# Optimization experiments

Measured on AMD Instinct MI355X. Metric: run time of the kernel, lower is better.

## Reference

```python
import jax, jax.numpy as jnp
import numpy as np

B, S, D = 4, 2048, 2048
H, NOPE, ROPE, V, KVR = 16, 128, 64, 128, 512
QK = NOPE + ROPE  # 192
THETA = 10000.0
EPS = 1e-6


def setup_inputs() -> dict:
    key = jax.random.key(0)
    ks = jax.random.split(key, 6)
    x = jax.random.normal(ks[0], (B, S, D), jnp.float32)
    wq = jax.random.normal(ks[1], (H * QK, D), jnp.float32) * 0.02
    wkv_a = jax.random.normal(ks[2], (KVR + ROPE, D), jnp.float32) * 0.02
    kv_norm_w = jnp.ones((KVR,), jnp.float32)
    wkv_b = jax.random.normal(ks[3], (H * (NOPE + V), KVR), jnp.float32) * 0.02
    wo = jax.random.normal(ks[4], (D, H * V), jnp.float32) * 0.02
    # rotary frequency tables (interleaved-pair convention, pairs = ROPE//2)
    pos = np.arange(S, dtype=np.float64)
    inv = 1.0 / (THETA ** (np.arange(0, ROPE, 2, dtype=np.float64) / ROPE))
    ang = pos[:, None] * inv[None, :]  # [S, ROPE//2]
    freqs_cos = jnp.asarray(np.cos(ang), jnp.float32)
    freqs_sin = jnp.asarray(np.sin(ang), jnp.float32)
    return dict(x=x, wq=wq, wkv_a=wkv_a, kv_norm_w=kv_norm_w,
                wkv_b=wkv_b, wo=wo, freqs_cos=freqs_cos, freqs_sin=freqs_sin)


def _rope(x, cos, sin):
    # x: [B, S, H, d] with interleaved complex pairs along last dim
    x1, x2 = x[..., 0::2], x[..., 1::2]
    c = cos[None, :, None, :]
    s = sin[None, :, None, :]
    y1 = x1 * c - x2 * s
    y2 = x1 * s + x2 * c
    return jnp.stack([y1, y2], axis=-1).reshape(x.shape)


def _rmsnorm(x, w):
    var = jnp.mean(jnp.square(x), axis=-1, keepdims=True)
    return x * jax.lax.rsqrt(var + EPS) * w


def reference(x, wq, wkv_a, kv_norm_w, wkv_b, wo, freqs_cos, freqs_sin):
    softmax_scale = QK ** (-0.5)  # mscale path inactive (S <= original_seq_len)
    # query projection (q_lora_rank == 0 -> direct)
    q = (x @ wq.T).reshape(B, S, H, QK)
    q_nope, q_pe = q[..., :NOPE], q[..., NOPE:]
    q_pe = _rope(q_pe, freqs_cos, freqs_sin)
    # latent KV projection + decoupled rope key
    kv = x @ wkv_a.T  # [B, S, KVR + ROPE]
    kv_c = _rmsnorm(kv[..., :KVR], kv_norm_w)  # latent KV cache entries
    k_pe = _rope(kv[..., None, KVR:], freqs_cos, freqs_sin)[:, :, 0]  # [B,S,ROPE]
    # absorb wkv_b's nope block into q (attention runs in 512-dim latent space)
    wkv_b_r = wkv_b.reshape(H, NOPE + V, KVR)
    q_lat = jnp.einsum('bshd,hdc->bshc', q_nope, wkv_b_r[:, :NOPE])
    scores = (jnp.einsum('bshc,btc->bsht', q_lat, kv_c)
              + jnp.einsum('bshr,btr->bsht', q_pe, k_pe)) * softmax_scale
    mask = jnp.triu(jnp.full((S, S), -1e9, jnp.float32), k=1)  # causal
    attn = jax.nn.softmax(scores + mask[None, :, None, :], axis=-1)
    out = jnp.einsum('bsht,btc->bshc', attn, kv_c)  # latent output
    out = jnp.einsum('bshc,hdc->bshd', out, wkv_b_r[:, NOPE:])  # un-absorb V
    return out.reshape(B, S, H * V) @ wo.T
```

## Files before the change

### kernel.cpp

```cpp
#include <hip/hip_runtime.h>
#include <hip/hip_bf16.h>
#include <cstdint>

typedef __bf16 bf16;
typedef __bf16 bf16x8 __attribute__((ext_vector_type(8)));
typedef float f32x4 __attribute__((ext_vector_type(4)));
typedef unsigned int u32x4 __attribute__((ext_vector_type(4)));

#define B_ 4
#define S_ 2048
#define D_ 2048
#define H_ 16
#define NOPE_ 128
#define ROPE_ 64
#define V_ 128
#define KVR_ 512
#define QK_ 192
#define KD_ 576

__device__ __forceinline__ bf16 tobf(float f) {
  unsigned u = __float_as_uint(f);
  u += 0x7fffu + ((u >> 16) & 1u);
  unsigned short s = (unsigned short)(u >> 16);
  return *reinterpret_cast<bf16*>(&s);
}
__device__ __forceinline__ float tof(bf16 v) {
  unsigned short s = *reinterpret_cast<unsigned short*>(&v);
  return __uint_as_float(((unsigned)s) << 16);
}

__global__ void cast_bf16(const float* __restrict__ in, bf16* __restrict__ out, long n) {
  long i = ((long)blockIdx.x * 256 + threadIdx.x) * 8;
  if (i >= n) return;
  float4 a = *(const float4*)(in + i);
  float4 b = *(const float4*)(in + i + 4);
  bf16x8 v;
  v[0] = tobf(a.x); v[1] = tobf(a.y); v[2] = tobf(a.z); v[3] = tobf(a.w);
  v[4] = tobf(b.x); v[5] = tobf(b.y); v[6] = tobf(b.z); v[7] = tobf(b.w);
  *(bf16x8*)(out + i) = v;
}

__global__ void prep_wkvb(const float* __restrict__ w, bf16* __restrict__ wnT, bf16* __restrict__ wv) {
  int tid = blockIdx.x * 256 + threadIdx.x;
  {
    int c = tid & 511, rest = tid >> 9, d = rest & 127, h = rest >> 7;
    wv[tid] = tobf(w[((long)(h * 256 + 128 + d) << 9) + c]);
  }
  {
    int d = tid & 127, rest = tid >> 7, c = rest & 511, h = rest >> 9;
    wnT[tid] = tobf(w[((long)(h * 256 + d) << 9) + c]);
  }
}

template <typename OutT>
__global__ __launch_bounds__(256)
void gemm_bt(const bf16* __restrict__ A, long lda, long aOffZ,
             const bf16* __restrict__ Bm, long ldb, long bOffZ,
             OutT* __restrict__ C, long ldc, long cOffZ,
             int M, int N, int K)
{
  A += aOffZ * blockIdx.z;
  Bm += bOffZ * blockIdx.z;
  C += cOffZ * blockIdx.z;
  const int m0 = blockIdx.y * 128, n0 = blockIdx.x * 128;
  const int tid = threadIdx.x;
  const int wave = tid >> 6, lane = tid & 63, quad = lane >> 4, r = lane & 15;
  const int wm = (wave >> 1) * 64, wn = (wave & 1) * 64;
  __shared__ __align__(16) bf16 As[128][40];
  __shared__ __align__(16) bf16 Bs[128][40];
  f32x4 acc[4][4] = {};
  for (int k0 = 0; k0 < K; k0 += 32) {
    __syncthreads();
#pragma unroll
    for (int it = 0; it < 2; ++it) {
      int idx = tid + it * 256;
      int row = idx >> 2, ch = (idx & 3) * 8;
      long ar = m0 + row; if (ar > (long)M - 1) ar = M - 1;
      *(u32x4*)&As[row][ch] = *(const u32x4*)(A + ar * lda + k0 + ch);
      long br = n0 + row; if (br > (long)N - 1) br = N - 1;
      *(u32x4*)&Bs[row][ch] = *(const u32x4*)(Bm + br * ldb + k0 + ch);
    }
    __syncthreads();
    bf16x8 af[4], bfr[4];
#pragma unroll
    for (int i = 0; i < 4; ++i) af[i] = *(const bf16x8*)&As[wm + i * 16 + r][quad * 8];
#pragma unroll
    for (int j = 0; j < 4; ++j) bfr[j] = *(const bf16x8*)&Bs[wn + j * 16 + r][quad * 8];
#pragma unroll
    for (int i = 0; i < 4; ++i)
#pragma unroll
      for (int j = 0; j < 4; ++j)
        acc[i][j] = __builtin_amdgcn_mfma_f32_16x16x32_bf16(af[i], bfr[j], acc[i][j], 0, 0, 0);
  }
#pragma unroll
  for (int i = 0; i < 4; ++i) {
    int mrow = m0 + wm + i * 16 + quad * 4;
#pragma unroll
    for (int j = 0; j < 4; ++j) {
      int ncol = n0 + wn + j * 16 + r;
      if (ncol < N) {
#pragma unroll
        for (int t = 0; t < 4; ++t) {
          if (mrow + t < M) {
            if constexpr (__is_same(OutT, float))
              C[(long)(mrow + t) * ldc + ncol] = acc[i][j][t];
            else
              C[(long)(mrow + t) * ldc + ncol] = tobf(acc[i][j][t]);
          }
        }
      }
    }
  }
}

__global__ void kv_norm(const float* __restrict__ kvf, const float* __restrict__ w,
                        const float* __restrict__ fcos, const float* __restrict__ fsin,
                        bf16* __restrict__ keff) {
  int row = blockIdx.x * 4 + (threadIdx.x >> 6);
  int lane = threadIdx.x & 63;
  int t = row;
  const float* src = kvf + (long)row * KD_;
  float v[8]; float ss = 0.f;
#pragma unroll
  for (int i = 0; i < 8; ++i) { v[i] = src[lane * 8 + i]; ss += v[i] * v[i]; }
#pragma unroll
  for (int off = 1; off < 64; off <<= 1) ss += __shfl_xor(ss, off, 64);
  float rms = rsqrtf(ss * (1.f / 512.f) + 1e-6f);
  bf16* dst = keff + (long)row * KD_;
#pragma unroll
  for (int i = 0; i < 8; ++i) dst[lane * 8 + i] = tobf(v[i] * rms * w[lane * 8 + i]);
  if (lane < 32) {
    float x1 = src[KVR_ + 2 * lane], x2 = src[KVR_ + 2 * lane + 1];
    float c = fcos[t * 32 + lane], s = fsin[t * 32 + lane];
    dst[KVR_ + 2 * lane]     = tobf(x1 * c - x2 * s);
    dst[KVR_ + 2 * lane + 1] = tobf(x1 * s + x2 * c);
  }
}

__global__ void transpose_kvc(const bf16* __restrict__ keff, bf16* __restrict__ kvcT) {
  int c0 = blockIdx.y * 32, t0 = blockIdx.x * 32;
  __shared__ bf16 tile[32][33];
  int x = threadIdx.x & 31, y = threadIdx.x >> 5;
#pragma unroll
  for (int k = 0; k < 4; ++k) {
    int t = t0 + y + k * 8;
    tile[y + k * 8][x] = keff[(long)t * KD_ + c0 + x];
  }
  __syncthreads();
#pragma unroll
  for (int k = 0; k < 4; ++k) {
    int c = c0 + y + k * 8;
    kvcT[(long)c * S_ + t0 + x] = tile[x][y + k * 8];
  }
}

__global__ void rope_q(const bf16* __restrict__ qb, const float* __restrict__ fcos,
                       const float* __restrict__ fsin, bf16* __restrict__ qeff) {
  long tid = (long)blockIdx.x * 256 + threadIdx.x;
  int i = tid & 31; int h = (tid >> 5) & 15; long bs = tid >> 9; int t = (int)bs;
  const bf16* src = qb + bs * (H_ * QK_) + h * QK_ + NOPE_ + 2 * i;
  float x1 = tof(src[0]), x2 = tof(src[1]);
  float c = fcos[t * 32 + i], s = fsin[t * 32 + i];
  long o = (bs * H_ + h) * KD_ + KVR_ + 2 * i;
  qeff[o]     = tobf(x1 * c - x2 * s);
  qeff[o + 1] = tobf(x1 * s + x2 * c);
}

__global__ __launch_bounds__(256, 2)
void flash_mla(const bf16* __restrict__ Qeff, const bf16* __restrict__ Keff,
               const bf16* __restrict__ kvcT, bf16* __restrict__ Oc)
{
  const int pair = blockIdx.x & 31, h = blockIdx.x >> 5;
  const int tid = threadIdx.x;
  const int wave = tid >> 6, lane = tid & 63, quad = lane >> 4, r = lane & 15;
  const int rowHalf = wave & 1, colHalf = wave >> 1;
  const int cbase = colHalf * 256;

  __shared__ __align__(16) bf16 Ks[32][584];
  __shared__ __align__(16) bf16 Vs[512][36];
  __shared__ __align__(16) bf16 Pl[2][16][40];
  const float scale = 0.07216878364870323f;

#pragma unroll 1
  for (int phase = 0; phase < 2; ++phase) {
    const int qt = phase ? (63 - pair) : pair;
    const int s0 = qt * 32;
    const int r0 = s0 + rowHalf * 16;
    const int nt = qt + 1;

    bf16x8 aq[18];
    const bf16* qrow = Qeff + ((long)(r0 + r) * H_ + h) * KD_;
#pragma unroll
    for (int kc = 0; kc < 18; ++kc) aq[kc] = *(const bf16x8*)(qrow + kc * 32 + quad * 8);

    f32x4 o[16] = {};
    float mrow[4], lrow[4];
#pragma unroll
    for (int t = 0; t < 4; ++t) { mrow[t] = -INFINITY; lrow[t] = 0.f; }

    for (int kt = 0; kt < nt; ++kt) {
      const int t0 = kt * 32;
      __syncthreads();
#pragma unroll
      for (int i = 0; i < 9; ++i) {
        int c = tid + i * 256;
        int row = c / 72, col = c - row * 72;
        *(u32x4*)&Ks[row][col * 8] = *(const u32x4*)(Keff + (long)(t0 + row) * KD_ + col * 8);
      }
#pragma unroll
      for (int i = 0; i < 8; ++i) {
        int c = tid + i * 256;
        int row = c >> 2, col = c & 3;
        *(u32x4*)&Vs[row][col * 8] = *(const u32x4*)(kvcT + (long)row * S_ + t0 + col * 8);
      }
      __syncthreads();
      f32x4 sacc[2] = {};
#pragma unroll
      for (int kc = 0; kc < 18; ++kc) {
        bf16x8 b0 = *(const bf16x8*)&Ks[r][kc * 32 + quad * 8];
        bf16x8 b1 = *(const bf16x8*)&Ks[16 + r][kc * 32 + quad * 8];
        sacc[0] = __builtin_amdgcn_mfma_f32_16x16x32_bf16(aq[kc], b0, sacc[0], 0, 0, 0);
        sacc[1] = __builtin_amdgcn_mfma_f32_16x16x32_bf16(aq[kc], b1, sacc[1], 0, 0, 0);
      }
      float alpha4[4];
#pragma unroll
      for (int tt = 0; tt < 4; ++tt) {
        int srow = r0 + quad * 4 + tt;
        float s0v = sacc[0][tt] * scale;
        float s1v = sacc[1][tt] * scale;
        s0v = (t0 + r <= srow) ? s0v : -INFINITY;
        s1v = (t0 + 16 + r <= srow) ? s1v : -INFINITY;
        float mx = fmaxf(s0v, s1v);
#pragma unroll
        for (int off = 1; off < 16; off <<= 1) mx = fmaxf(mx, __shfl_xor(mx, off, 64));
        float mnew = fmaxf(mrow[tt], mx);
        float al = __expf(mrow[tt] - mnew);
        float p0 = __expf(s0v - mnew);
        float p1 = __expf(s1v - mnew);
        float rs = p0 + p1;
#pragma unroll
        for (int off = 1; off < 16; off <<= 1) rs += __shfl_xor(rs, off, 64);
        lrow[tt] = lrow[tt] * al + rs;
        mrow[tt] = mnew;
        alpha4[tt] = al;
        if (wave < 2) {
          Pl[rowHalf][quad * 4 + tt][r]      = tobf(p0);
          Pl[rowHalf][quad * 4 + tt][16 + r] = tobf(p1);
        }
      }
#pragma unroll
      for (int j = 0; j < 16; ++j) {
#pragma unroll
        for (int tt = 0; tt < 4; ++tt) o[j][tt] *= alpha4[tt];
      }
      __syncthreads();
      bf16x8 pa = *(const bf16x8*)&Pl[rowHalf][r][quad * 8];
#pragma unroll
      for (int j = 0; j < 16; ++j) {
        bf16x8 bv = *(const bf16x8*)&Vs[cbase + j * 16 + r][quad * 8];
        o[j] = __builtin_amdgcn_mfma_f32_16x16x32_bf16(pa, bv, o[j], 0, 0, 0);
      }
    }
#pragma unroll
    for (int tt = 0; tt < 4; ++tt) {
      long srow = (long)(r0 + quad * 4 + tt);
      bf16* orow = Oc + (srow * H_ + h) * KVR_ + cbase;
      float li = 1.0f / lrow[tt];
#pragma unroll
      for (int j = 0; j < 16; ++j) orow[j * 16 + r] = tobf(o[j][tt] * li);
    }
  }
}

extern "C" void kernel_launch(void* const* d_in, const int* in_sizes, int n_in,
                              void* d_out, int out_size, void* d_ws, size_t ws_size,
                              hipStream_t stream) {
  (void)in_sizes; (void)n_in; (void)out_size; (void)ws_size;
  const float* x     = (const float*)d_in[0];
  const float* wq    = (const float*)d_in[1];
  const float* wkv_a = (const float*)d_in[2];
  const float* kvw   = (const float*)d_in[3];
  const float* wkv_b = (const float*)d_in[4];
  const float* wo    = (const float*)d_in[5];
  const float* fcos  = (const float*)d_in[6];
  const float* fsin  = (const float*)d_in[7];
  float* out = (float*)d_out;

  char* p = (char*)d_ws;
  auto alloc = [&](size_t bytes) { char* q = p; p += (bytes + 255) & ~(size_t)255; return q; };
  const long MR = (long)B_ * S_;
  bf16* xb   = (bf16*)alloc(MR * D_ * 2);
  bf16* out2 = (bf16*)alloc(MR * D_ * 2);
  bf16* wqb  = (bf16*)alloc((long)H_ * QK_ * D_ * 2);
  bf16* wab  = (bf16*)alloc((long)KD_ * D_ * 2);
  bf16* wob  = (bf16*)alloc((long)D_ * D_ * 2);
  bf16* wbnT = (bf16*)alloc((long)H_ * KVR_ * NOPE_ * 2);
  bf16* wbv  = (bf16*)alloc((long)H_ * V_ * KVR_ * 2);
  float* kvf = (float*)alloc((long)S_ * KD_ * 4);
  bf16* keff = (bf16*)alloc((long)S_ * KD_ * 2);
  bf16* kvcT = (bf16*)alloc((long)KVR_ * S_ * 2);
  bf16* qb   = (bf16*)alloc((long)S_ * H_ * QK_ * 2);
  bf16* qeff = (bf16*)alloc((long)S_ * H_ * KD_ * 2);
  bf16* oc   = (bf16*)alloc((long)S_ * H_ * KVR_ * 2);

  cast_bf16<<<(MR * D_) >> 11, 256, 0, stream>>>(x, xb, MR * D_);
  cast_bf16<<<((long)H_ * QK_ * D_) >> 11, 256, 0, stream>>>(wq, wqb, (long)H_ * QK_ * D_);
  cast_bf16<<<((long)KD_ * D_) >> 11, 256, 0, stream>>>(wkv_a, wab, (long)KD_ * D_);
  cast_bf16<<<((long)D_ * D_) >> 11, 256, 0, stream>>>(wo, wob, (long)D_ * D_);
  prep_wkvb<<<4096, 256, 0, stream>>>(wkv_b, wbnT, wbv);

  for (int b = 0; b < B_; ++b) {
    const bf16* xb_b = xb + (long)b * S_ * D_;
    bf16* out2_b = out2 + (long)b * S_ * D_;
    gemm_bt<float><<<dim3(5, 16, 1), 256, 0, stream>>>(xb_b, D_, 0, wab, D_, 0,
                                                       kvf, KD_, 0, S_, KD_, D_);
    kv_norm<<<S_ / 4, 256, 0, stream>>>(kvf, kvw, fcos, fsin, keff);
    transpose_kvc<<<dim3(S_ / 32, KVR_ / 32, 1), 256, 0, stream>>>(keff, kvcT);
    gemm_bt<bf16><<<dim3(24, 16, 1), 256, 0, stream>>>(xb_b, D_, 0, wqb, D_, 0,
                                                       qb, H_ * QK_, 0, S_, H_ * QK_, D_);
    rope_q<<<(S_ * H_ * 32) / 256, 256, 0, stream>>>(qb, fcos, fsin, qeff);
    gemm_bt<bf16><<<dim3(4, 16, H_), 256, 0, stream>>>(qb, H_ * QK_, QK_,
                                                       wbnT, NOPE_, (long)KVR_ * NOPE_,
                                                       qeff, H_ * KD_, KD_, S_, KVR_, NOPE_);
    flash_mla<<<dim3(512), 256, 0, stream>>>(qeff, keff, kvcT, oc);
    gemm_bt<bf16><<<dim3(1, 16, H_), 256, 0, stream>>>(oc, H_ * KVR_, KVR_,
                                                       wbv, KVR_, (long)V_ * KVR_,
                                                       out2_b, D_, V_, S_, V_, KVR_);
  }
  gemm_bt<float><<<dim3(16, 64, 1), 256, 0, stream>>>(out2, D_, 0, wob, D_, 0,
                                                      out, D_, 0, MR, D_, D_);
}
```

Baseline: 2.579 ms.

## Process 64-row query tiles per block with transposed score MFMA in flash_mla

```diff
diff --git a/kernel.cpp b/kernel.cpp
--- a/kernel.cpp
+++ b/kernel.cpp
@@ -170,104 +170,113 @@
 void flash_mla(const bf16* __restrict__ Qeff, const bf16* __restrict__ Keff,
                const bf16* __restrict__ kvcT, bf16* __restrict__ Oc)
 {
-  const int pair = blockIdx.x & 31, h = blockIdx.x >> 5;
+  const int qt = 31 - (blockIdx.x >> 4);
+  const int h = blockIdx.x & 15;
+  const int s0 = qt * 64;
   const int tid = threadIdx.x;
   const int wave = tid >> 6, lane = tid & 63, quad = lane >> 4, r = lane & 15;
-  const int rowHalf = wave & 1, colHalf = wave >> 1;
-  const int cbase = colHalf * 256;
+  const int rh = wave & 1, ch = wave >> 1;
+  const int nt = 2 * qt + 2;
 
   __shared__ __align__(16) bf16 Ks[32][584];
   __shared__ __align__(16) bf16 Vs[512][36];
-  __shared__ __align__(16) bf16 Pl[2][16][40];
+  __shared__ __align__(16) bf16 Pl[64][36];
+  __shared__ __align__(16) float alphaL[64];
+  __shared__ __align__(16) float linvL[64];
   const float scale = 0.07216878364870323f;
 
-#pragma unroll 1
-  for (int phase = 0; phase < 2; ++phase) {
-    const int qt = phase ? (63 - pair) : pair;
-    const int s0 = qt * 32;
-    const int r0 = s0 + rowHalf * 16;
-    const int nt = qt + 1;
-
-    bf16x8 aq[18];
-    const bf16* qrow = Qeff + ((long)(r0 + r) * H_ + h) * KD_;
-#pragma unroll
-    for (int kc = 0; kc < 18; ++kc) aq[kc] = *(const bf16x8*)(qrow + kc * 32 + quad * 8);
-
-    f32x4 o[16] = {};
-    float mrow[4], lrow[4];
-#pragma unroll
-    for (int t = 0; t < 4; ++t) { mrow[t] = -INFINITY; lrow[t] = 0.f; }
-
-    for (int kt = 0; kt < nt; ++kt) {
-      const int t0 = kt * 32;
-      __syncthreads();
-#pragma unroll
-      for (int i = 0; i < 9; ++i) {
-        int c = tid + i * 256;
-        int row = c / 72, col = c - row * 72;
-        *(u32x4*)&Ks[row][col * 8] = *(const u32x4*)(Keff + (long)(t0 + row) * KD_ + col * 8);
-      }
-#pragma unroll
-      for (int i = 0; i < 8; ++i) {
-        int c = tid + i * 256;
-        int row = c >> 2, col = c & 3;
-        *(u32x4*)&Vs[row][col * 8] = *(const u32x4*)(kvcT + (long)row * S_ + t0 + col * 8);
-      }
-      __syncthreads();
-      f32x4 sacc[2] = {};
-#pragma unroll
-      for (int kc = 0; kc < 18; ++kc) {
-        bf16x8 b0 = *(const bf16x8*)&Ks[r][kc * 32 + quad * 8];
-        bf16x8 b1 = *(const bf16x8*)&Ks[16 + r][kc * 32 + quad * 8];
-        sacc[0] = __builtin_amdgcn_mfma_f32_16x16x32_bf16(aq[kc], b0, sacc[0], 0, 0, 0);
-        sacc[1] = __builtin_amdgcn_mfma_f32_16x16x32_bf16(aq[kc], b1, sacc[1], 0, 0, 0);
-      }
-      float alpha4[4];
-#pragma unroll
-      for (int tt = 0; tt < 4; ++tt) {
-        int srow = r0 + quad * 4 + tt;
-        float s0v = sacc[0][tt] * scale;
-        float s1v = sacc[1][tt] * scale;
-        s0v = (t0 + r <= srow) ? s0v : -INFINITY;
-        s1v = (t0 + 16 + r <= srow) ? s1v : -INFINITY;
-        float mx = fmaxf(s0v, s1v);
-#pragma unroll
-        for (int off = 1; off < 16; off <<= 1) mx = fmaxf(mx, __shfl_xor(mx, off, 64));
-        float mnew = fmaxf(mrow[tt], mx);
-        float al = __expf(mrow[tt] - mnew);
-        float p0 = __expf(s0v - mnew);
-        float p1 = __expf(s1v - mnew);
-        float rs = p0 + p1;
-#pragma unroll
-        for (int off = 1; off < 16; off <<= 1) rs += __shfl_xor(rs, off, 64);
-        lrow[tt] = lrow[tt] * al + rs;
-        mrow[tt] = mnew;
-        alpha4[tt] = al;
-        if (wave < 2) {
-          Pl[rowHalf][quad * 4 + tt][r]      = tobf(p0);
-          Pl[rowHalf][quad * 4 + tt][16 + r] = tobf(p1);
-        }
-      }
-#pragma unroll
-      for (int j = 0; j < 16; ++j) {
-#pragma unroll
-        for (int tt = 0; tt < 4; ++tt) o[j][tt] *= alpha4[tt];
-      }
-      __syncthreads();
-      bf16x8 pa = *(const bf16x8*)&Pl[rowHalf][r][quad * 8];
-#pragma unroll
-      for (int j = 0; j < 16; ++j) {
-        bf16x8 bv = *(const bf16x8*)&Vs[cbase + j * 16 + r][quad * 8];
-        o[j] = __builtin_amdgcn_mfma_f32_16x16x32_bf16(pa, bv, o[j], 0, 0, 0);
-      }
-    }
+  const int qrow = s0 + 16 * wave + r;
+  bf16x8 aq[18];
+  const bf16* qptr = Qeff + ((long)qrow * H_ + h) * KD_;
+#pragma unroll
+  for (int kc = 0; kc < 18; ++kc) aq[kc] = *(const bf16x8*)(qptr + kc * 32 + quad * 8);
+
+  f32x4 o0[16] = {};
+  f32x4 o1[16] = {};
+  float m_run = -INFINITY, l_run = 0.f;
+
+  for (int kt = 0; kt < nt; ++kt) {
+    const int t0 = kt * 32;
+    __syncthreads();
+#pragma unroll
+    for (int i = 0; i < 9; ++i) {
+      int c = tid + i * 256;
+      int row = c / 72, col = c - row * 72;
+      *(u32x4*)&Ks[row][col * 8] = *(const u32x4*)(Keff + (long)(t0 + row) * KD_ + col * 8);
+    }
+#pragma unroll
+    for (int i = 0; i < 8; ++i) {
+      int c = tid + i * 256;
+      int row = c >> 2, col = c & 3;
+      *(u32x4*)&Vs[row][col * 8] = *(const u32x4*)(kvcT + (long)row * S_ + t0 + col * 8);
+    }
+    __syncthreads();
+    f32x4 sacc0 = {}, sacc1 = {};
+#pragma unroll
+    for (int kc = 0; kc < 18; ++kc) {
+      bf16x8 k0 = *(const bf16x8*)&Ks[r][kc * 32 + quad * 8];
+      bf16x8 k1 = *(const bf16x8*)&Ks[16 + r][kc * 32 + quad * 8];
+      sacc0 = __builtin_amdgcn_mfma_f32_16x16x32_bf16(k0, aq[kc], sacc0, 0, 0, 0);
+      sacc1 = __builtin_amdgcn_mfma_f32_16x16x32_bf16(k1, aq[kc], sacc1, 0, 0, 0);
+    }
+    float s8[8];
 #pragma unroll
     for (int tt = 0; tt < 4; ++tt) {
-      long srow = (long)(r0 + quad * 4 + tt);
-      bf16* orow = Oc + (srow * H_ + h) * KVR_ + cbase;
-      float li = 1.0f / lrow[tt];
-#pragma unroll
-      for (int j = 0; j < 16; ++j) orow[j * 16 + r] = tobf(o[j][tt] * li);
+      int ka = t0 + quad * 4 + tt;
+      s8[tt]     = (ka      <= qrow) ? sacc0[tt] * scale : -INFINITY;
+      s8[4 + tt] = (ka + 16 <= qrow) ? sacc1[tt] * scale : -INFINITY;
+    }
+    float mx = s8[0];
+#pragma unroll
+    for (int i = 1; i < 8; ++i) mx = fmaxf(mx, s8[i]);
+    mx = fmaxf(mx, __shfl_xor(mx, 16, 64));
+    mx = fmaxf(mx, __shfl_xor(mx, 32, 64));
+    float mnew = fmaxf(m_run, mx);
+    float alpha = __expf(m_run - mnew);
+    float ps = 0.f;
+#pragma unroll
+    for (int i = 0; i < 8; ++i) { float pv = __expf(s8[i] - mnew); s8[i] = pv; ps += pv; }
+    ps += __shfl_xor(ps, 16, 64);
+    ps += __shfl_xor(ps, 32, 64);
+    l_run = l_run * alpha + ps;
+    m_run = mnew;
+#pragma unroll
+    for (int tt = 0; tt < 4; ++tt) {
+      Pl[16 * wave + r][quad * 4 + tt]      = tobf(s8[tt]);
+      Pl[16 * wave + r][16 + quad * 4 + tt] = tobf(s8[4 + tt]);
+    }
+    if (quad == 0) alphaL[16 * wave + r] = alpha;
+    __syncthreads();
+    f32x4 a0 = *(const f32x4*)&alphaL[32 * rh + quad * 4];
+    f32x4 a1 = *(const f32x4*)&alphaL[32 * rh + 16 + quad * 4];
+#pragma unroll
+    for (int j = 0; j < 16; ++j) {
+#pragma unroll
+      for (int tt = 0; tt < 4; ++tt) { o0[j][tt] *= a0[tt]; o1[j][tt] *= a1[tt]; }
+    }
+    bf16x8 p0 = *(const bf16x8*)&Pl[32 * rh + r][quad * 8];
+    bf16x8 p1 = *(const bf16x8*)&Pl[32 * rh + 16 + r][quad * 8];
+#pragma unroll
+    for (int j = 0; j < 16; ++j) {
+      bf16x8 bv = *(const bf16x8*)&Vs[256 * ch + 16 * j + r][quad * 8];
+      o0[j] = __builtin_amdgcn_mfma_f32_16x16x32_bf16(p0, bv, o0[j], 0, 0, 0);
+      o1[j] = __builtin_amdgcn_mfma_f32_16x16x32_bf16(p1, bv, o1[j], 0, 0, 0);
+    }
+  }
+  if (quad == 0) linvL[16 * wave + r] = 1.0f / l_run;
+  __syncthreads();
+  f32x4 li0 = *(const f32x4*)&linvL[32 * rh + quad * 4];
+  f32x4 li1 = *(const f32x4*)&linvL[32 * rh + 16 + quad * 4];
+#pragma unroll
+  for (int tt = 0; tt < 4; ++tt) {
+    long row0 = (long)(s0 + 32 * rh + quad * 4 + tt);
+    long row1 = row0 + 16;
+    bf16* orow0 = Oc + (row0 * H_ + h) * KVR_ + 256 * ch;
+    bf16* orow1 = Oc + (row1 * H_ + h) * KVR_ + 256 * ch;
+#pragma unroll
+    for (int j = 0; j < 16; ++j) {
+      orow0[j * 16 + r] = tobf(o0[j][tt] * li0[tt]);
+      orow1[j * 16 + r] = tobf(o1[j][tt] * li1[tt]);
     }
   }
 }
```

New measurement: 2.595 ms. No clear change (+0.6%).
